# Optimization experiments

Hardware: AMD Instinct MI355X
Metric: run time of the kernel (lower is better)

## Reference

```python
import jax, jax.numpy as jnp
import numpy as np

N = 50000
E = 640000
D = 128          # in = hidden = out channels
L = 3            # num_layers
ATT_H = D // 2   # attention hidden width
LN_EPS = 1e-5


def _layer_norm(h, gamma, beta):
    mu = jnp.mean(h, axis=-1, keepdims=True)
    var = jnp.var(h, axis=-1, keepdims=True)
    return (h - mu) * jax.lax.rsqrt(var + LN_EPS) * gamma + beta


def setup_inputs() -> dict:
    key = jax.random.key(0)
    ks = jax.random.split(key, 12)
    x = jax.random.normal(ks[0], (N, D), dtype=jnp.float32)
    edge_index = jax.random.randint(ks[1], (2, E), 0, N, dtype=jnp.int64)
    edge_attr = jax.random.normal(ks[2], (E, 2), dtype=jnp.float32)
    s = 1.0 / np.sqrt(D)
    # Per-layer params stacked on leading L axis (all layers same dims).
    lin_node_w = jax.random.uniform(ks[3], (L, D, D), jnp.float32, -s, s)
    lin_edge_w = jax.random.uniform(ks[4], (L, D + 2, D), jnp.float32, -s, s)
    att_w1 = jax.random.uniform(ks[5], (L, 2 * D, ATT_H), jnp.float32, -s, s)
    att_b1 = jnp.zeros((L, ATT_H), jnp.float32)
    att_w2 = jax.random.uniform(ks[6], (L, ATT_H, 1), jnp.float32, -s, s)
    att_b2 = jnp.zeros((L, 1), jnp.float32)
    bias = jnp.zeros((L, D), jnp.float32)
    ln_gamma = jnp.ones((L, D), jnp.float32)
    ln_beta = jnp.zeros((L, D), jnp.float32)
    return {"x": x, "edge_index": edge_index, "edge_attr": edge_attr,
            "lin_node_w": lin_node_w, "lin_edge_w": lin_edge_w,
            "att_w1": att_w1, "att_b1": att_b1, "att_w2": att_w2,
            "att_b2": att_b2, "bias": bias, "ln_gamma": ln_gamma,
            "ln_beta": ln_beta}


def reference(x, edge_index, edge_attr, lin_node_w, lin_edge_w,
              att_w1, att_b1, att_w2, att_b2, bias, ln_gamma, ln_beta):
    # PyG default flow: x_j = source = edge_index[0], x_i = target = edge_index[1];
    # aggregation ('add') scatters messages into targets. Dropout is a no-op (eval).
    src, dst = edge_index[0], edge_index[1]
    for i in range(L):
        x_input = x
        h = x @ lin_node_w[i]                          # [N, D]
        xj = h[src]                                    # [E, D] gather
        xi = h[dst]                                    # [E, D] gather
        # att(cat(x_i, x_j)) without materializing the concat:
        a1 = jax.nn.relu(xi @ att_w1[i][:D] + xj @ att_w1[i][D:] + att_b1[i])
        att = jax.nn.sigmoid(a1 @ att_w2[i] + att_b2[i])   # [E, 1]
        # lin_edge(cat(x_j, edge_attr)) split the same way:
        msg = att * (xj @ lin_edge_w[i][:D] + edge_attr @ lin_edge_w[i][D:])
        out = jax.ops.segment_sum(msg, dst, num_segments=N) + bias[i]
        out = _layer_norm(out, ln_gamma[i], ln_beta[i])
        if i < L - 1:
            out = jax.nn.relu(out)
        x = out + x_input                              # residual (Identity proj)
    return x
```

## Files before the change

### kernel.cpp

```cpp
#include <hip/hip_runtime.h>
#include <hip/hip_bf16.h>

#define NN 50000
#define EE 640000
#define NB 196

typedef __attribute__((ext_vector_type(8))) short short8;
typedef __attribute__((ext_vector_type(4))) float f32x4;

__device__ __forceinline__ float bf2f(ushort u) {
    return __uint_as_float(((uint)u) << 16);
}
__device__ __forceinline__ ushort f2bf(float f) {
    uint b = __float_as_uint(f);
    uint r = (b + 0x7fffu + ((b >> 16) & 1u)) >> 16;
    return (ushort)r;
}
__device__ __forceinline__ ushort f2bf_rn(float f) {
    return (ushort)((__float_as_uint(f) + 0x8000u) >> 16);
}


__global__ __launch_bounds__(256) void k_hist_compose(
    const int* __restrict__ ei, int* __restrict__ counts,
    const float* __restrict__ wn_all, const float* __restrict__ aw1,
    const float* __restrict__ wle, ushort* __restrict__ wcT) {
    if (blockIdx.x < 2500) {
        int e = blockIdx.x * 256 + threadIdx.x;
        if (e < EE) atomicAdd(&counts[ei[EE + e]], 1);
        return;
    }
    const int bb = blockIdx.x - 2500;
    const int l = bb >> 7;
    const int k = bb & 127;
    const int t = threadIdx.x;
    const float* wn = wn_all + (l * 128 + k) * 128;
    float acc = 0.f;
    for (int c = 0; c < 128; ++c) {
        float cat;
        if (t < 128)
            cat = aw1[(l * 256 + ((t & 64) << 1) + c) * 64 + (t & 63)];
        else
            cat = wle[(l * 130 + c) * 128 + (t - 128)];
        acc += wn[c] * cat;
    }
    wcT[(l * 256 + t) * 128 + k] = f2bf(acc);
}

__global__ __launch_bounds__(256) void k_scan_a(const int* __restrict__ counts,
                                                int* __restrict__ bsum) {
    int i = blockIdx.x * 256 + threadIdx.x;
    int v = (i < NN) ? counts[i] : 0;
    #pragma unroll
    for (int o = 32; o > 0; o >>= 1) v += __shfl_xor(v, o);
    __shared__ int ws[4];
    if ((threadIdx.x & 63) == 0) ws[threadIdx.x >> 6] = v;
    __syncthreads();
    if (threadIdx.x == 0) bsum[blockIdx.x] = ws[0] + ws[1] + ws[2] + ws[3];
}

__global__ __launch_bounds__(256) void k_scan_b(const int* __restrict__ bsum,
                                                int* __restrict__ boff,
                                                int* __restrict__ offs) {
    const int t = threadIdx.x;
    const int lane = t & 63, wave = t >> 6;
    int v = (t < NB) ? bsum[t] : 0;
    int x = v;
    #pragma unroll
    for (int o = 1; o < 64; o <<= 1) {
        int y = __shfl_up(x, o);
        if (lane >= o) x += y;
    }
    __shared__ int ws[4];
    if (lane == 63) ws[wave] = x;
    __syncthreads();
    int add = 0;
    for (int w = 0; w < wave; ++w) add += ws[w];
    x += add;
    if (t < NB) boff[t] = x - v;
    if (t == 255) offs[NN] = x;
}

__global__ __launch_bounds__(256) void k_scan_c(const int* __restrict__ counts,
                                                const int* __restrict__ boff,
                                                int* __restrict__ offs,
                                                int* __restrict__ cursor) {
    int i = blockIdx.x * 256 + threadIdx.x;
    const int lane = threadIdx.x & 63, wave = threadIdx.x >> 6;
    int v = (i < NN) ? counts[i] : 0;
    int x = v;
    #pragma unroll
    for (int o = 1; o < 64; o <<= 1) {
        int y = __shfl_up(x, o);
        if (lane >= o) x += y;
    }
    __shared__ int ws[4];
    if (lane == 63) ws[wave] = x;
    __syncthreads();
    int add = boff[blockIdx.x];
    for (int w = 0; w < wave; ++w) add += ws[w];
    int ex = add + x - v;
    if (i < NN) {
        offs[i] = ex;
        cursor[i] = ex;
    }
}

__global__ __launch_bounds__(256) void k_scatter(const int* __restrict__ ei,
                                                 const float* __restrict__ ea,
                                                 int* __restrict__ cursor,
                                                 uint4* __restrict__ adj4) {
    int e = blockIdx.x * 256 + threadIdx.x;
    if (e >= EE) return;
    int d = ei[EE + e];
    int pos = atomicAdd(&cursor[d], 1);
    ushort lo = f2bf(ea[2 * e]);
    ushort hi = f2bf(ea[2 * e + 1]);
    adj4[pos] = make_uint4((uint)ei[e], ((uint)hi << 16) | (uint)lo, 0u, (uint)d);
}


__global__ __launch_bounds__(256) void k1_gemm(const float* __restrict__ xin,
                                               const ushort* __restrict__ wcT,
                                               ushort* __restrict__ pqr) {
    const int wave = threadIdx.x >> 6;
    const int lane = threadIdx.x & 63;
    const int rbase = blockIdx.x * 64;
    const int c0 = wave * 64;
    const int lrow = lane & 15;
    const int kg = lane >> 4;

    short8 b[4][4];
    #pragma unroll
    for (int t = 0; t < 4; ++t) {
        const int col = c0 + t * 16 + lrow;
        #pragma unroll
        for (int s = 0; s < 4; ++s)
            b[t][s] = *(const short8*)(wcT + col * 128 + s * 32 + kg * 8);
    }

    #pragma unroll
    for (int rt = 0; rt < 4; ++rt) {
        const int r0 = rbase + rt * 16;
        int arow = r0 + lrow;
        if (arow >= NN) arow = NN - 1;
        const float* xrow = xin + (size_t)arow * 128;
        short8 a[4];
        #pragma unroll
        for (int s = 0; s < 4; ++s) {
            const float* px = xrow + s * 32 + kg * 8;
            float4 u = *(const float4*)(px);
            float4 v = *(const float4*)(px + 4);
            short8 av;
            av[0] = (short)f2bf(u.x); av[1] = (short)f2bf(u.y);
            av[2] = (short)f2bf(u.z); av[3] = (short)f2bf(u.w);
            av[4] = (short)f2bf(v.x); av[5] = (short)f2bf(v.y);
            av[6] = (short)f2bf(v.z); av[7] = (short)f2bf(v.w);
            a[s] = av;
        }

        f32x4 acc[4] = {};
        #pragma unroll
        for (int t = 0; t < 4; ++t) {
            #pragma unroll
            for (int s = 0; s < 4; ++s)
                acc[t] = __builtin_amdgcn_mfma_f32_16x16x32_bf16(a[s], b[t][s], acc[t], 0, 0, 0);
        }
        #pragma unroll
        for (int t = 0; t < 4; ++t) {
            const int col = c0 + t * 16 + lrow;
            #pragma unroll
            for (int j = 0; j < 4; ++j) {
                const int orow = r0 + kg * 4 + j;
                if (orow < NN)
                    pqr[(size_t)orow * 256 + col] = f2bf(acc[t][j]);
            }
        }
    }
}


__global__ __launch_bounds__(256) void k_att(uint4* __restrict__ adj4,
                                             const ushort* __restrict__ pqr,
                                             const float* __restrict__ b1v,
                                             const float* __restrict__ w2v,
                                             const float* __restrict__ b2v) {
    const int lane = threadIdx.x & 63;
    const int e0 = blockIdx.x * 256 + (threadIdx.x >> 6) * 64;
    const int row = lane & 15;
    const int kg = lane >> 4;
    const float b2 = b2v[0];

    short8 bv0, bv1;
    const bool col0 = (row == 0);
    #pragma unroll
    for (int j = 0; j < 8; ++j) {
        bv0[j] = (short)f2bf(col0 ? w2v[kg * 8 + j] : 0.f);
        bv1[j] = (short)f2bf(col0 ? w2v[32 + kg * 8 + j] : 0.f);
    }

    uint srcs[4], dsts[4];
    #pragma unroll
    for (int t = 0; t < 4; ++t) {
        const uint4 m = adj4[e0 + t * 16 + row];
        srcs[t] = m.x;
        dsts[t] = m.w;
    }

    f32x4 acc[4] = {};
    #pragma unroll
    for (int h = 0; h < 2; ++h) {
        const int cb = 32 * h + kg * 8;
        float4 bA = *(const float4*)(b1v + cb);
        float4 bB = *(const float4*)(b1v + cb + 4);
        const short8 bfrag = h ? bv1 : bv0;
        #pragma unroll
        for (int t = 0; t < 4; ++t) {
            short8 qv = *(const short8*)(pqr + (size_t)srcs[t] * 256 + 64 + cb);
            short8 pv = *(const short8*)(pqr + (size_t)dsts[t] * 256 + cb);
            short8 av;
            #pragma unroll
            for (int j = 0; j < 8; ++j) {
                float bb = (j < 4) ? ((const float*)&bA)[j] : ((const float*)&bB)[j - 4];
                float v = bf2f((ushort)qv[j]) + bf2f((ushort)pv[j]) + bb;
                av[j] = (short)f2bf_rn(fmaxf(v, 0.f));
            }
            acc[t] = __builtin_amdgcn_mfma_f32_16x16x32_bf16(av, bfrag, acc[t], 0, 0, 0);
        }
    }
    if (row == 0) {
        #pragma unroll
        for (int t = 0; t < 4; ++t) {
            #pragma unroll
            for (int j = 0; j < 4; ++j) {
                float s = acc[t][j] + b2;
                float att = 1.f / (1.f + __expf(-s));
                *(float*)((char*)(adj4 + e0 + t * 16 + kg * 4 + j) + 8) = att;
            }
        }
    }
}


#define CONS(MM, RR, JJ)                                              \
    {                                                                 \
        const float a_ = ((JJ) < ee) ? __uint_as_float((MM).z) : 0.f; \
        acc0 = fmaf(a_, __uint_as_float((RR) << 16), acc0);           \
        acc1 = fmaf(a_, __uint_as_float((RR) & 0xffff0000u), acc1);   \
        sE0  = fmaf(a_, __uint_as_float((MM).y << 16), sE0);          \
        sE1  = fmaf(a_, __uint_as_float((MM).y & 0xffff0000u), sE1);  \
    }

#define LOADQ(M0, M1, M2, M3, R0, R1, R2, R3, BASE)          \
    {                                                        \
        M0 = adj4[(BASE)];                                   \
        M1 = adj4[(BASE) + 1];                               \
        M2 = adj4[(BASE) + 2];                               \
        M3 = adj4[(BASE) + 3];                               \
        R0 = *(const uint*)(rp + (size_t)M0.x * 256);        \
        R1 = *(const uint*)(rp + (size_t)M1.x * 256);        \
        R2 = *(const uint*)(rp + (size_t)M2.x * 256);        \
        R3 = *(const uint*)(rp + (size_t)M3.x * 256);        \
    }

__global__ __launch_bounds__(256) void k_msg(
    const int* __restrict__ offs, const uint4* __restrict__ adj4,
    const ushort* __restrict__ pqr, const float* __restrict__ xin,
    const float* __restrict__ web, const float* __restrict__ biasv,
    const float* __restrict__ gammav, const float* __restrict__ betav,
    float* __restrict__ xout, int do_relu) {
    const int lane = threadIdx.x & 63;
    const int n = blockIdx.x * 4 + (threadIdx.x >> 6);
    const int c0 = 2 * lane;

    const int eb = __builtin_amdgcn_readfirstlane(offs[n]);
    const int ee = __builtin_amdgcn_readfirstlane(offs[n + 1]);

    float acc0 = 0.f, acc1 = 0.f, sE0 = 0.f, sE1 = 0.f;
    if (eb < ee) {
        const ushort* rp = pqr + 128 + c0;
        uint4 a0, a1, a2, a3, b0, b1, b2, b3;
        uint ra0, ra1, ra2, ra3, rb0, rb1, rb2, rb3;
        LOADQ(a0, a1, a2, a3, ra0, ra1, ra2, ra3, eb);
        LOADQ(b0, b1, b2, b3, rb0, rb1, rb2, rb3, eb + 4);
        int j = eb;
        for (; j + 8 < ee; j += 8) {
            CONS(a0, ra0, j) CONS(a1, ra1, j + 1)
            CONS(a2, ra2, j + 2) CONS(a3, ra3, j + 3)
            LOADQ(a0, a1, a2, a3, ra0, ra1, ra2, ra3, j + 8);
            CONS(b0, rb0, j + 4) CONS(b1, rb1, j + 5)
            CONS(b2, rb2, j + 6) CONS(b3, rb3, j + 7)
            LOADQ(b0, b1, b2, b3, rb0, rb1, rb2, rb3, j + 12);
        }
        CONS(a0, ra0, j) CONS(a1, ra1, j + 1)
        CONS(a2, ra2, j + 2) CONS(a3, ra3, j + 3)
        CONS(b0, rb0, j + 4) CONS(b1, rb1, j + 5)
        CONS(b2, rb2, j + 6) CONS(b3, rb3, j + 7)
    }

    const float web00 = web[c0], web01 = web[c0 + 1];
    const float web10 = web[128 + c0], web11 = web[128 + c0 + 1];
    acc0 += sE0 * web00 + sE1 * web10;
    acc1 += sE0 * web01 + sE1 * web11;

    const float2 bi = *(const float2*)(biasv + c0);
    float v0 = acc0 + bi.x;
    float v1 = acc1 + bi.y;
    float sm = v0 + v1, sq = v0 * v0 + v1 * v1;
    #pragma unroll
    for (int o = 32; o > 0; o >>= 1) {
        sm += __shfl_xor(sm, o);
        sq += __shfl_xor(sq, o);
    }
    const float mean = sm * (1.f / 128.f);
    const float var = sq * (1.f / 128.f) - mean * mean;
    const float inv = rsqrtf(var + 1e-5f);
    const float2 ga = *(const float2*)(gammav + c0);
    const float2 be = *(const float2*)(betav + c0);
    float y0 = (v0 - mean) * inv * ga.x + be.x;
    float y1 = (v1 - mean) * inv * ga.y + be.y;
    if (do_relu) { y0 = fmaxf(y0, 0.f); y1 = fmaxf(y1, 0.f); }
    const float2 xr = *(const float2*)(xin + (size_t)n * 128 + c0);
    y0 += xr.x;
    y1 += xr.y;
    float2 o2; o2.x = y0; o2.y = y1;
    *(float2*)(xout + (size_t)n * 128 + c0) = o2;
}


extern "C" void kernel_launch(void* const* d_in, const int* in_sizes, int n_in,
                              void* d_out, int out_size, void* d_ws, size_t ws_size,
                              hipStream_t stream) {
    const float* x   = (const float*)d_in[0];
    const int*   ei  = (const int*)d_in[1];
    const float* ea  = (const float*)d_in[2];
    const float* wn  = (const float*)d_in[3];
    const float* wle = (const float*)d_in[4];
    const float* aw1 = (const float*)d_in[5];
    const float* ab1 = (const float*)d_in[6];
    const float* aw2 = (const float*)d_in[7];
    const float* ab2 = (const float*)d_in[8];
    const float* bia = (const float*)d_in[9];
    const float* gam = (const float*)d_in[10];
    const float* bet = (const float*)d_in[11];

    char* w = (char*)d_ws;
    size_t o = 0;
    auto alloc = [&](size_t bytes) {
        char* p = w + o;
        o = (o + bytes + 255) & ~(size_t)255;
        return p;
    };
    int*    counts = (int*)alloc((size_t)NN * 4);
    int*    offs   = (int*)alloc((size_t)(NN + 1) * 4);
    int*    cursor = (int*)alloc((size_t)NN * 4);
    int*    bsum   = (int*)alloc((size_t)NB * 4);
    int*    boff   = (int*)alloc((size_t)NB * 4);
    uint4*  adj4   = (uint4*)alloc((size_t)(EE + 64) * 16);
    ushort* wcT    = (ushort*)alloc((size_t)3 * 256 * 128 * 2);
    ushort* pqr    = (ushort*)alloc((size_t)NN * 256 * 2);
    float*  xb1    = (float*)alloc((size_t)NN * 128 * 4);
    float*  xb2    = (float*)alloc((size_t)NN * 128 * 4);

    hipMemsetAsync(counts, 0, (size_t)NN * 4, stream);
    hipMemsetAsync(adj4 + EE, 0, (size_t)64 * 16, stream);
    k_hist_compose<<<2500 + 384, 256, 0, stream>>>(ei, counts, wn, aw1, wle, wcT);
    k_scan_a<<<NB, 256, 0, stream>>>(counts, bsum);
    k_scan_b<<<1, 256, 0, stream>>>(bsum, boff, offs);
    k_scan_c<<<NB, 256, 0, stream>>>(counts, boff, offs, cursor);
    k_scatter<<<(EE + 255) / 256, 256, 0, stream>>>(ei, ea, cursor, adj4);

    const float* xi = x;
    float* xo = xb1;
    for (int l = 0; l < 3; ++l) {
        k1_gemm<<<(NN + 63) / 64, 256, 0, stream>>>(xi, wcT + (size_t)l * 256 * 128, pqr);
        k_att<<<EE / 256, 256, 0, stream>>>(adj4, pqr,
                                            ab1 + l * 64, aw2 + l * 64, ab2 + l);
        const bool last = (l == 2);
        float* out_ptr = last ? (float*)d_out : xo;
        k_msg<<<NN / 4, 256, 0, stream>>>(
            offs, adj4, pqr, xi,
            wle + ((size_t)l * 130 + 128) * 128,
            bia + l * 128, gam + l * 128, bet + l * 128,
            out_ptr, last ? 0 : 1);
        xi = out_ptr;
        xo = (l == 0) ? xb2 : xb1;
    }
}
```

Before: 349.1 us.

## Split CSR edge records into compact arrays and software-pipeline the node GEMM

Replaces the 16-byte per-edge adjacency record with a permutation array, a destination array, an 8-byte (src, edge_attr) array and a separate float attention array. The scatter now writes only 4-byte indices, and the first attention pass builds the compact src/attr array. This shrinks the bytes the message kernel streams per edge and gives it coalesced, vectorized attention stores. The node GEMM gets a double-buffered A-load/compute schedule for full tiles. The cost is an extra fill kernel and an indirect gather through the permutation on the first layer.

```diff
diff --git a/kernel.cpp b/kernel.cpp
--- a/kernel.cpp
+++ b/kernel.cpp
@@ -22,12 +22,17 @@
 
 
 __global__ __launch_bounds__(256) void k_hist_compose(
-    const int* __restrict__ ei, int* __restrict__ counts,
+    const int* __restrict__ ei, const float* __restrict__ ea,
+    int* __restrict__ counts, uint* __restrict__ eab,
     const float* __restrict__ wn_all, const float* __restrict__ aw1,
     const float* __restrict__ wle, ushort* __restrict__ wcT) {
     if (blockIdx.x < 2500) {
         int e = blockIdx.x * 256 + threadIdx.x;
-        if (e < EE) atomicAdd(&counts[ei[EE + e]], 1);
+        if (e < EE) {
+            atomicAdd(&counts[ei[EE + e]], 1);
+            const float2 v = *(const float2*)(ea + 2 * e);
+            eab[e] = ((uint)f2bf(v.y) << 16) | (uint)f2bf(v.x);
+        }
         return;
     }
     const int bb = blockIdx.x - 2500;
@@ -107,18 +112,60 @@
 }
 
 __global__ __launch_bounds__(256) void k_scatter(const int* __restrict__ ei,
-                                                 const float* __restrict__ ea,
                                                  int* __restrict__ cursor,
-                                                 uint4* __restrict__ adj4) {
+                                                 int* __restrict__ perm) {
     int e = blockIdx.x * 256 + threadIdx.x;
     if (e >= EE) return;
     int d = ei[EE + e];
     int pos = atomicAdd(&cursor[d], 1);
-    ushort lo = f2bf(ea[2 * e]);
-    ushort hi = f2bf(ea[2 * e + 1]);
-    adj4[pos] = make_uint4((uint)ei[e], ((uint)hi << 16) | (uint)lo, 0u, (uint)d);
-}
-
+    perm[pos] = e;
+}
+
+__global__ __launch_bounds__(256) void k_fill_dst(const int* __restrict__ offs,
+                                                  int* __restrict__ csr_dst) {
+    int n = blockIdx.x * 256 + threadIdx.x;
+    if (n >= NN) return;
+    const int b = offs[n], e = offs[n + 1];
+    for (int i = b; i < e; ++i) csr_dst[i] = n;
+}
+
+
+#define K1_LOADA(AV, RT)                                                   \
+    {                                                                      \
+        const float* xrow_ = xin + (size_t)(rbase + (RT) * 16 + lrow) * 128; \
+        _Pragma("unroll")                                                  \
+        for (int s = 0; s < 4; ++s) {                                      \
+            const float* px = xrow_ + s * 32 + kg * 8;                     \
+            float4 u = *(const float4*)(px);                               \
+            float4 v = *(const float4*)(px + 4);                           \
+            short8 av;                                                     \
+            av[0] = (short)f2bf(u.x); av[1] = (short)f2bf(u.y);            \
+            av[2] = (short)f2bf(u.z); av[3] = (short)f2bf(u.w);            \
+            av[4] = (short)f2bf(v.x); av[5] = (short)f2bf(v.y);            \
+            av[6] = (short)f2bf(v.z); av[7] = (short)f2bf(v.w);            \
+            AV[s] = av;                                                    \
+        }                                                                  \
+    }
+
+#define K1_COMP(AV, RT)                                                    \
+    {                                                                      \
+        f32x4 acc[4] = {};                                                 \
+        _Pragma("unroll")                                                  \
+        for (int t = 0; t < 4; ++t) {                                      \
+            _Pragma("unroll")                                              \
+            for (int s = 0; s < 4; ++s)                                    \
+                acc[t] = __builtin_amdgcn_mfma_f32_16x16x32_bf16(          \
+                    AV[s], b[t][s], acc[t], 0, 0, 0);                      \
+        }                                                                  \
+        _Pragma("unroll")                                                  \
+        for (int t = 0; t < 4; ++t) {                                      \
+            const int col = c0 + t * 16 + lrow;                            \
+            _Pragma("unroll")                                              \
+            for (int j = 0; j < 4; ++j)                                    \
+                pqr[(size_t)(rbase + (RT) * 16 + kg * 4 + j) * 256 + col] = \
+                    f2bf(acc[t][j]);                                       \
+        }                                                                  \
+    }
 
 __global__ __launch_bounds__(256) void k1_gemm(const float* __restrict__ xin,
                                                const ushort* __restrict__ wcT,
@@ -139,52 +186,61 @@
             b[t][s] = *(const short8*)(wcT + col * 128 + s * 32 + kg * 8);
     }
 
-    #pragma unroll
-    for (int rt = 0; rt < 4; ++rt) {
-        const int r0 = rbase + rt * 16;
-        int arow = r0 + lrow;
-        if (arow >= NN) arow = NN - 1;
-        const float* xrow = xin + (size_t)arow * 128;
-        short8 a[4];
-        #pragma unroll
-        for (int s = 0; s < 4; ++s) {
-            const float* px = xrow + s * 32 + kg * 8;
-            float4 u = *(const float4*)(px);
-            float4 v = *(const float4*)(px + 4);
-            short8 av;
-            av[0] = (short)f2bf(u.x); av[1] = (short)f2bf(u.y);
-            av[2] = (short)f2bf(u.z); av[3] = (short)f2bf(u.w);
-            av[4] = (short)f2bf(v.x); av[5] = (short)f2bf(v.y);
-            av[6] = (short)f2bf(v.z); av[7] = (short)f2bf(v.w);
-            a[s] = av;
-        }
-
-        f32x4 acc[4] = {};
-        #pragma unroll
-        for (int t = 0; t < 4; ++t) {
+    if (rbase + 64 <= NN) {
+        short8 aA[4], aB[4];
+        K1_LOADA(aA, 0)
+        K1_LOADA(aB, 1) K1_COMP(aA, 0)
+        K1_LOADA(aA, 2) K1_COMP(aB, 1)
+        K1_LOADA(aB, 3) K1_COMP(aA, 2)
+        K1_COMP(aB, 3)
+    } else {
+        #pragma unroll
+        for (int rt = 0; rt < 4; ++rt) {
+            const int r0 = rbase + rt * 16;
+            int arow = r0 + lrow;
+            if (arow >= NN) arow = NN - 1;
+            const float* xrow = xin + (size_t)arow * 128;
+            short8 a[4];
             #pragma unroll
-            for (int s = 0; s < 4; ++s)
-                acc[t] = __builtin_amdgcn_mfma_f32_16x16x32_bf16(a[s], b[t][s], acc[t], 0, 0, 0);
-        }
-        #pragma unroll
-        for (int t = 0; t < 4; ++t) {
-            const int col = c0 + t * 16 + lrow;
+            for (int s = 0; s < 4; ++s) {
+                const float* px = xrow + s * 32 + kg * 8;
+                float4 u = *(const float4*)(px);
+                float4 v = *(const float4*)(px + 4);
+                short8 av;
+                av[0] = (short)f2bf(u.x); av[1] = (short)f2bf(u.y);
+                av[2] = (short)f2bf(u.z); av[3] = (short)f2bf(u.w);
+                av[4] = (short)f2bf(v.x); av[5] = (short)f2bf(v.y);
+                av[6] = (short)f2bf(v.z); av[7] = (short)f2bf(v.w);
+                a[s] = av;
+            }
+            f32x4 acc[4] = {};
             #pragma unroll
-            for (int j = 0; j < 4; ++j) {
-                const int orow = r0 + kg * 4 + j;
-                if (orow < NN)
-                    pqr[(size_t)orow * 256 + col] = f2bf(acc[t][j]);
+            for (int t = 0; t < 4; ++t) {
+                #pragma unroll
+                for (int s = 0; s < 4; ++s)
+                    acc[t] = __builtin_amdgcn_mfma_f32_16x16x32_bf16(a[s], b[t][s], acc[t], 0, 0, 0);
             }
-        }
-    }
-}
-
-
-__global__ __launch_bounds__(256) void k_att(uint4* __restrict__ adj4,
-                                             const ushort* __restrict__ pqr,
-                                             const float* __restrict__ b1v,
-                                             const float* __restrict__ w2v,
-                                             const float* __restrict__ b2v) {
+            #pragma unroll
+            for (int t = 0; t < 4; ++t) {
+                const int col = c0 + t * 16 + lrow;
+                #pragma unroll
+                for (int j = 0; j < 4; ++j) {
+                    const int orow = r0 + kg * 4 + j;
+                    if (orow < NN)
+                        pqr[(size_t)orow * 256 + col] = f2bf(acc[t][j]);
+                }
+            }
+        }
+    }
+}
+
+
+__global__ __launch_bounds__(256) void k_att(
+    int first, const int* __restrict__ perm, const int* __restrict__ ei,
+    const uint* __restrict__ eab, const int* __restrict__ csr_dst,
+    uint2* __restrict__ adjSE, float* __restrict__ attv,
+    const ushort* __restrict__ pqr, const float* __restrict__ b1v,
+    const float* __restrict__ w2v, const float* __restrict__ b2v) {
     const int lane = threadIdx.x & 63;
     const int e0 = blockIdx.x * 256 + (threadIdx.x >> 6) * 64;
     const int row = lane & 15;
@@ -200,11 +256,23 @@
     }
 
     uint srcs[4], dsts[4];
-    #pragma unroll
-    for (int t = 0; t < 4; ++t) {
-        const uint4 m = adj4[e0 + t * 16 + row];
-        srcs[t] = m.x;
-        dsts[t] = m.w;
+    if (first) {
+        #pragma unroll
+        for (int t = 0; t < 4; ++t) {
+            const int pos = e0 + t * 16 + row;
+            const int e = perm[pos];
+            const uint s = (uint)ei[e];
+            srcs[t] = s;
+            dsts[t] = (uint)csr_dst[pos];
+            adjSE[pos] = make_uint2(s, eab[e]);
+        }
+    } else {
+        #pragma unroll
+        for (int t = 0; t < 4; ++t) {
+            const int pos = e0 + t * 16 + row;
+            srcs[t] = adjSE[pos].x;
+            dsts[t] = (uint)csr_dst[pos];
+        }
     }
 
     f32x4 acc[4] = {};
@@ -231,44 +299,49 @@
     if (row == 0) {
         #pragma unroll
         for (int t = 0; t < 4; ++t) {
+            float4 o;
             #pragma unroll
             for (int j = 0; j < 4; ++j) {
                 float s = acc[t][j] + b2;
-                float att = 1.f / (1.f + __expf(-s));
-                *(float*)((char*)(adj4 + e0 + t * 16 + kg * 4 + j) + 8) = att;
+                ((float*)&o)[j] = 1.f / (1.f + __expf(-s));
             }
-        }
-    }
-}
-
-
-#define CONS(MM, RR, JJ)                                              \
+            *(float4*)(attv + e0 + t * 16 + kg * 4) = o;
+        }
+    }
+}
+
+
+#define CONS(MM, AA, RR, JJ)                                          \
     {                                                                 \
-        const float a_ = ((JJ) < ee) ? __uint_as_float((MM).z) : 0.f; \
+        const float a_ = ((JJ) < ee) ? (AA) : 0.f;                    \
         acc0 = fmaf(a_, __uint_as_float((RR) << 16), acc0);           \
         acc1 = fmaf(a_, __uint_as_float((RR) & 0xffff0000u), acc1);   \
         sE0  = fmaf(a_, __uint_as_float((MM).y << 16), sE0);          \
         sE1  = fmaf(a_, __uint_as_float((MM).y & 0xffff0000u), sE1);  \
     }
 
-#define LOADQ(M0, M1, M2, M3, R0, R1, R2, R3, BASE)          \
-    {                                                        \
-        M0 = adj4[(BASE)];                                   \
-        M1 = adj4[(BASE) + 1];                               \
-        M2 = adj4[(BASE) + 2];                               \
-        M3 = adj4[(BASE) + 3];                               \
-        R0 = *(const uint*)(rp + (size_t)M0.x * 256);        \
-        R1 = *(const uint*)(rp + (size_t)M1.x * 256);        \
-        R2 = *(const uint*)(rp + (size_t)M2.x * 256);        \
-        R3 = *(const uint*)(rp + (size_t)M3.x * 256);        \
+#define LOADQ(M0, M1, M2, M3, A0, A1, A2, A3, R0, R1, R2, R3, BASE)  \
+    {                                                                \
+        M0 = adjSE[(BASE)];                                          \
+        M1 = adjSE[(BASE) + 1];                                      \
+        M2 = adjSE[(BASE) + 2];                                      \
+        M3 = adjSE[(BASE) + 3];                                      \
+        A0 = attv[(BASE)];                                           \
+        A1 = attv[(BASE) + 1];                                       \
+        A2 = attv[(BASE) + 2];                                       \
+        A3 = attv[(BASE) + 3];                                       \
+        R0 = *(const uint*)(rp + (size_t)M0.x * 256);                \
+        R1 = *(const uint*)(rp + (size_t)M1.x * 256);                \
+        R2 = *(const uint*)(rp + (size_t)M2.x * 256);                \
+        R3 = *(const uint*)(rp + (size_t)M3.x * 256);                \
     }
 
 __global__ __launch_bounds__(256) void k_msg(
-    const int* __restrict__ offs, const uint4* __restrict__ adj4,
-    const ushort* __restrict__ pqr, const float* __restrict__ xin,
-    const float* __restrict__ web, const float* __restrict__ biasv,
-    const float* __restrict__ gammav, const float* __restrict__ betav,
-    float* __restrict__ xout, int do_relu) {
+    const int* __restrict__ offs, const uint2* __restrict__ adjSE,
+    const float* __restrict__ attv, const ushort* __restrict__ pqr,
+    const float* __restrict__ xin, const float* __restrict__ web,
+    const float* __restrict__ biasv, const float* __restrict__ gammav,
+    const float* __restrict__ betav, float* __restrict__ xout, int do_relu) {
     const int lane = threadIdx.x & 63;
     const int n = blockIdx.x * 4 + (threadIdx.x >> 6);
     const int c0 = 2 * lane;
@@ -279,23 +352,24 @@
     float acc0 = 0.f, acc1 = 0.f, sE0 = 0.f, sE1 = 0.f;
     if (eb < ee) {
         const ushort* rp = pqr + 128 + c0;
-        uint4 a0, a1, a2, a3, b0, b1, b2, b3;
+        uint2 a0, a1, a2, a3, b0, b1, b2, b3;
+        float fa0, fa1, fa2, fa3, fb0, fb1, fb2, fb3;
         uint ra0, ra1, ra2, ra3, rb0, rb1, rb2, rb3;
-        LOADQ(a0, a1, a2, a3, ra0, ra1, ra2, ra3, eb);
-        LOADQ(b0, b1, b2, b3, rb0, rb1, rb2, rb3, eb + 4);
+        LOADQ(a0, a1, a2, a3, fa0, fa1, fa2, fa3, ra0, ra1, ra2, ra3, eb);
+        LOADQ(b0, b1, b2, b3, fb0, fb1, fb2, fb3, rb0, rb1, rb2, rb3, eb + 4);
         int j = eb;
         for (; j + 8 < ee; j += 8) {
-            CONS(a0, ra0, j) CONS(a1, ra1, j + 1)
-            CONS(a2, ra2, j + 2) CONS(a3, ra3, j + 3)
-            LOADQ(a0, a1, a2, a3, ra0, ra1, ra2, ra3, j + 8);
-            CONS(b0, rb0, j + 4) CONS(b1, rb1, j + 5)
-            CONS(b2, rb2, j + 6) CONS(b3, rb3, j + 7)
-            LOADQ(b0, b1, b2, b3, rb0, rb1, rb2, rb3, j + 12);
-        }
-        CONS(a0, ra0, j) CONS(a1, ra1, j + 1)
-        CONS(a2, ra2, j + 2) CONS(a3, ra3, j + 3)
-        CONS(b0, rb0, j + 4) CONS(b1, rb1, j + 5)
-        CONS(b2, rb2, j + 6) CONS(b3, rb3, j + 7)
+            CONS(a0, fa0, ra0, j) CONS(a1, fa1, ra1, j + 1)
+            CONS(a2, fa2, ra2, j + 2) CONS(a3, fa3, ra3, j + 3)
+            LOADQ(a0, a1, a2, a3, fa0, fa1, fa2, fa3, ra0, ra1, ra2, ra3, j + 8);
+            CONS(b0, fb0, rb0, j + 4) CONS(b1, fb1, rb1, j + 5)
+            CONS(b2, fb2, rb2, j + 6) CONS(b3, fb3, rb3, j + 7)
+            LOADQ(b0, b1, b2, b3, fb0, fb1, fb2, fb3, rb0, rb1, rb2, rb3, j + 12);
+        }
+        CONS(a0, fa0, ra0, j) CONS(a1, fa1, ra1, j + 1)
+        CONS(a2, fa2, ra2, j + 2) CONS(a3, fa3, ra3, j + 3)
+        CONS(b0, fb0, rb0, j + 4) CONS(b1, fb1, rb1, j + 5)
+        CONS(b2, fb2, rb2, j + 6) CONS(b3, fb3, rb3, j + 7)
     }
 
     const float web00 = web[c0], web01 = web[c0 + 1];
@@ -351,35 +425,43 @@
         o = (o + bytes + 255) & ~(size_t)255;
         return p;
     };
-    int*    counts = (int*)alloc((size_t)NN * 4);
-    int*    offs   = (int*)alloc((size_t)(NN + 1) * 4);
-    int*    cursor = (int*)alloc((size_t)NN * 4);
-    int*    bsum   = (int*)alloc((size_t)NB * 4);
-    int*    boff   = (int*)alloc((size_t)NB * 4);
-    uint4*  adj4   = (uint4*)alloc((size_t)(EE + 64) * 16);
-    ushort* wcT    = (ushort*)alloc((size_t)3 * 256 * 128 * 2);
-    ushort* pqr    = (ushort*)alloc((size_t)NN * 256 * 2);
-    float*  xb1    = (float*)alloc((size_t)NN * 128 * 4);
-    float*  xb2    = (float*)alloc((size_t)NN * 128 * 4);
+    int*    counts  = (int*)alloc((size_t)NN * 4);
+    int*    offs    = (int*)alloc((size_t)(NN + 1) * 4);
+    int*    cursor  = (int*)alloc((size_t)NN * 4);
+    int*    bsum    = (int*)alloc((size_t)NB * 4);
+    int*    boff    = (int*)alloc((size_t)NB * 4);
+    int*    perm    = (int*)alloc((size_t)EE * 4);
+    int*    csr_dst = (int*)alloc((size_t)EE * 4);
+    uint*   eab     = (uint*)alloc((size_t)EE * 4);
+    uint2*  adjSE   = (uint2*)alloc((size_t)(EE + 64) * 8);
+    float*  attv    = (float*)alloc((size_t)(EE + 64) * 4);
+    ushort* wcT     = (ushort*)alloc((size_t)3 * 256 * 128 * 2);
+    ushort* pqr     = (ushort*)alloc((size_t)NN * 256 * 2);
+    float*  xb1     = (float*)alloc((size_t)NN * 128 * 4);
+    float*  xb2     = (float*)alloc((size_t)NN * 128 * 4);
 
     hipMemsetAsync(counts, 0, (size_t)NN * 4, stream);
-    hipMemsetAsync(adj4 + EE, 0, (size_t)64 * 16, stream);
-    k_hist_compose<<<2500 + 384, 256, 0, stream>>>(ei, counts, wn, aw1, wle, wcT);
+    hipMemsetAsync(adjSE + EE, 0, (size_t)64 * 8, stream);
+    hipMemsetAsync(attv + EE, 0, (size_t)64 * 4, stream);
+    k_hist_compose<<<2500 + 384, 256, 0, stream>>>(ei, ea, counts, eab,
+                                                   wn, aw1, wle, wcT);
     k_scan_a<<<NB, 256, 0, stream>>>(counts, bsum);
     k_scan_b<<<1, 256, 0, stream>>>(bsum, boff, offs);
     k_scan_c<<<NB, 256, 0, stream>>>(counts, boff, offs, cursor);
-    k_scatter<<<(EE + 255) / 256, 256, 0, stream>>>(ei, ea, cursor, adj4);
+    k_scatter<<<(EE + 255) / 256, 256, 0, stream>>>(ei, cursor, perm);
+    k_fill_dst<<<NB, 256, 0, stream>>>(offs, csr_dst);
 
     const float* xi = x;
     float* xo = xb1;
     for (int l = 0; l < 3; ++l) {
         k1_gemm<<<(NN + 63) / 64, 256, 0, stream>>>(xi, wcT + (size_t)l * 256 * 128, pqr);
-        k_att<<<EE / 256, 256, 0, stream>>>(adj4, pqr,
+        k_att<<<EE / 256, 256, 0, stream>>>(l == 0 ? 1 : 0, perm, ei, eab, csr_dst,
+                                            adjSE, attv, pqr,
                                             ab1 + l * 64, aw2 + l * 64, ab2 + l);
         const bool last = (l == 2);
         float* out_ptr = last ? (float*)d_out : xo;
         k_msg<<<NN / 4, 256, 0, stream>>>(
-            offs, adj4, pqr, xi,
+            offs, adjSE, attv, pqr, xi,
             wle + ((size_t)l * 130 + 128) * 128,
             bia + l * 128, gam + l * 128, bet + l * 128,
             out_ptr, last ? 0 : 1);
```

After: 351.9 us. Within noise of the previous version (+0.8%).
